# Performance work log

Hardware: AMD Instinct MI355X
Metric: run time of the kernel (lower is better)

## Reference

```python
import math
import jax, jax.numpy as jnp
import numpy as np

N, T, D, H, DH = 4, 2048, 1024, 16, 64
CAP = 30.0
EPS = 1e-5


def _layernorm(x, g, b):
    m = jnp.mean(x, axis=-1, keepdims=True)
    v = jnp.mean(jnp.square(x - m), axis=-1, keepdims=True)
    return (x - m) * jax.lax.rsqrt(v + EPS) * g + b


def _rope(x):
    # x: [N, H, t, d]; interleaved rotary (rotary-embedding-torch style), theta=10000
    t, d = x.shape[2], x.shape[3]
    inv_freq = 1.0 / (10000.0 ** (jnp.arange(0, d, 2, dtype=jnp.float32) / d))
    ang = jnp.arange(t, dtype=jnp.float32)[:, None] * inv_freq[None, :]  # [t, d/2]
    cos, sin = jnp.cos(ang), jnp.sin(ang)
    x1, x2 = x[..., 0::2], x[..., 1::2]
    r1 = x1 * cos - x2 * sin
    r2 = x1 * sin + x2 * cos
    return jnp.stack([r1, r2], axis=-1).reshape(x.shape)


def setup_inputs() -> dict:
    key = jax.random.key(0)
    ks = jax.random.split(key, 8)
    s = 0.02
    lengths = jax.random.randint(ks[6], (N,), T // 2, T + 1).astype(jnp.int32)
    key_padding_mask = jnp.arange(T)[None, :] >= lengths[:, None]  # True = pad
    attn_mask = jnp.triu(jnp.ones((T, T), dtype=bool), 1)  # causal: True = masked
    return {
        "x": jax.random.normal(ks[0], (N, T, D), jnp.float32),
        "ln_g": jnp.ones((D,), jnp.float32),
        "ln_b": jnp.zeros((D,), jnp.float32),
        "Wq": jax.random.normal(ks[1], (D, H * DH), jnp.float32) * s,
        "bq": jnp.zeros((H * DH,), jnp.float32),
        "Wk": jax.random.normal(ks[2], (D, H * DH), jnp.float32) * s,
        "bk": jnp.zeros((H * DH,), jnp.float32),
        "Wv": jax.random.normal(ks[3], (D, H * DH), jnp.float32) * s,
        "bv": jnp.zeros((H * DH,), jnp.float32),
        "Wo": jax.random.normal(ks[4], (H * DH, D), jnp.float32) * s,
        "bo": jnp.zeros((D,), jnp.float32),
        "key_padding_mask": key_padding_mask,
        "attn_mask": attn_mask,
        "key_value_sequence_lengths": lengths,
    }


def reference(x, ln_g, ln_b, Wq, bq, Wk, bk, Wv, bv, Wo, bo,
              key_padding_mask, attn_mask, key_value_sequence_lengths):
    n, t, _ = x.shape
    h = _layernorm(x, ln_g, ln_b)  # shared LN for q/k/v (self-attention)
    q = (h @ Wq + bq).reshape(n, t, H, DH).transpose(0, 2, 1, 3)  # [n,H,t,d]
    k = (h @ Wk + bk).reshape(n, t, H, DH).transpose(0, 2, 1, 3)
    v = (h @ Wv + bv).reshape(n, t, H, DH).transpose(0, 2, 1, 3)
    q = _rope(q)
    k = _rope(k)
    scores = jnp.einsum('bhtd,bhTd->bhtT', q, k) / math.sqrt(DH)
    scores = CAP * jnp.tanh(scores / CAP)  # tanh soft-cap
    mask = key_padding_mask[:, None, None, :] | attn_mask[None, None, :, :]
    scores = jnp.where(mask, -jnp.inf, scores)
    attn = jax.nn.softmax(scores, axis=-1)
    out = jnp.einsum('bhtT,bhTd->bhtd', attn, v)
    out = out.transpose(0, 2, 1, 3).reshape(n, t, H * DH)
    return out @ Wo + bo
```

## Files before the change

### kernel.cpp

```cpp
#include <hip/hip_runtime.h>
#include <hip/hip_bf16.h>

typedef unsigned short u16;
typedef unsigned int   u32;
typedef __bf16 bf16x8 __attribute__((ext_vector_type(8)));
typedef float  f32x4  __attribute__((ext_vector_type(4)));

#define NB 4
#define T_ 2048
#define D_ 1024
#define H_ 16
#define DH 64
#define M_ (NB * T_)
#define PSTR 72

__device__ __forceinline__ float bf2f(u16 u) {
    union { u32 i; float f; } v; v.i = ((u32)u) << 16; return v.f;
}
__device__ __forceinline__ u16 f2bf(float f) {
    union { float fl; u32 i; } v; v.fl = f;
    u32 r = v.i + 0x7fff + ((v.i >> 16) & 1);
    return (u16)(r >> 16);
}

__device__ __forceinline__ void gl_lds16(const u16* g, u16* l) {
    __builtin_amdgcn_global_load_lds((const __attribute__((address_space(1))) void*)g,
                                     (__attribute__((address_space(3))) void*)l,
                                     16, 0, 0);
}

__device__ __forceinline__ int detect_f32(const u16* p) {
    int weird = 0;
    const int lane = threadIdx.x & 63;
    #pragma unroll
    for (int i = 0; i < 4; ++i) {
        const u16 u = p[lane * 4 + i];
        const int e = (u >> 7) & 0xFF;
        weird += (e == 0xFF || (e >= 0x01 && e <= 0x3F) || (e >= 0xC0 && e <= 0xFE));
    }
    #pragma unroll
    for (int off = 32; off; off >>= 1) weird += __shfl_xor(weird, off);
    return weird >= 16;
}

__device__ __forceinline__ int read_len(const void* raw, int b) {
    const int* a32 = (const int*)raw;
    bool ok32 = true;
    #pragma unroll
    for (int i = 0; i < NB; ++i) {
        const int v = a32[i];
        if (v < 1 || v > T_) ok32 = false;
    }
    int v = ok32 ? a32[b] : (int)((const long long*)raw)[b];
    return min(max(v, 1), T_);
}

__global__ __launch_bounds__(256) void prep_kernel(const void* __restrict__ xraw,
                                                   const void* __restrict__ graw,
                                                   const void* __restrict__ braw,
                                                   u16* __restrict__ h,
                                                   const void* __restrict__ W0,
                                                   const void* __restrict__ W1,
                                                   const void* __restrict__ W2,
                                                   const void* __restrict__ W3,
                                                   u16* __restrict__ Wt0,
                                                   u16* __restrict__ Wt1,
                                                   u16* __restrict__ Wt2,
                                                   u16* __restrict__ Wt3,
                                                   float2* __restrict__ tab) {
    __shared__ __align__(16) u16 sh[64 * PSTR];
    const int bid = blockIdx.x;
    const int tid = threadIdx.x;

    if (bid < M_) {
        const int row = bid;
        const int isf = detect_f32((const u16*)xraw);
        float* red = (float*)sh;

        float xv[4];
        if (isf) {
            const float* xr = (const float*)xraw + (size_t)row * D_;
            *(float4*)xv = *(const float4*)&xr[tid * 4];
        } else {
            const u16* xr = (const u16*)xraw + (size_t)row * D_;
            u16 loc[4] __attribute__((aligned(8)));
            *(uint2*)loc = *(const uint2*)&xr[tid * 4];
            #pragma unroll
            for (int i = 0; i < 4; ++i) xv[i] = bf2f(loc[i]);
        }

        float s = xv[0] + xv[1] + xv[2] + xv[3];
        float q = xv[0]*xv[0] + xv[1]*xv[1] + xv[2]*xv[2] + xv[3]*xv[3];
        #pragma unroll
        for (int off = 32; off; off >>= 1) {
            s += __shfl_xor(s, off);
            q += __shfl_xor(q, off);
        }
        const int wave = tid >> 6, lane = tid & 63;
        if (lane == 0) { red[wave] = s; red[4 + wave] = q; }
        __syncthreads();
        s = red[0] + red[1] + red[2] + red[3];
        q = red[4] + red[5] + red[6] + red[7];

        const float mean = s * (1.0f / D_);
        const float var  = q * (1.0f / D_) - mean * mean;
        const float rs   = rsqrtf(var + 1e-5f);

        u16 o[4] __attribute__((aligned(8)));
        #pragma unroll
        for (int i = 0; i < 4; ++i) {
            const int c = tid * 4 + i;
            const float gv = isf ? ((const float*)graw)[c] : bf2f(((const u16*)graw)[c]);
            const float bv = isf ? ((const float*)braw)[c] : bf2f(((const u16*)braw)[c]);
            o[i] = f2bf((xv[i] - mean) * rs * gv + bv);
        }
        *(uint2*)&h[(size_t)row * D_ + tid * 4] = *(uint2*)o;
    } else if (bid < M_ + 1024) {
        const int w = bid - M_;
        const int z = w >> 8;
        const int t = w & 255;
        const void* Wraw = (z == 0) ? W0 : (z == 1) ? W1 : (z == 2) ? W2 : W3;
        u16* Wt          = (z == 0) ? Wt0 : (z == 1) ? Wt1 : (z == 2) ? Wt2 : Wt3;
        u16 (*tile)[PSTR] = (u16(*)[PSTR])sh;
        const int isf = detect_f32((const u16*)Wraw);
        const int n0 = (t & 15) * 64;
        const int k0 = (t >> 4) * 64;
        const int tr  = tid >> 2;
        const int tc  = (tid & 3) * 16;

        if (isf) {
            const float* W = (const float*)Wraw;
            #pragma unroll
            for (int i = 0; i < 16; ++i)
                tile[tc + i][tr] = f2bf(W[(size_t)(k0 + tr) * D_ + n0 + tc + i]);
        } else {
            const u16* W = (const u16*)Wraw;
            #pragma unroll
            for (int i = 0; i < 16; ++i)
                tile[tc + i][tr] = W[(size_t)(k0 + tr) * D_ + n0 + tc + i];
        }
        __syncthreads();
        *(uint4*)&Wt[(size_t)(n0 + tr) * D_ + k0 + tc]     = *(uint4*)&tile[tr][tc];
        *(uint4*)&Wt[(size_t)(n0 + tr) * D_ + k0 + tc + 8] = *(uint4*)&tile[tr][tc + 8];
    } else {
        const int gid = (bid - (M_ + 1024)) * 256 + tid;
        const int t = gid >> 5, i = gid & 31;
        const float inv = exp2f(-(float)i * 0.41524101186092f);
        const float ang = (float)t * inv;
        float sv, cv;
        sincosf(ang, &sv, &cv);
        tab[gid] = make_float2(cv, sv);
    }
}

__global__ __launch_bounds__(256) void wconv_kernel(const void* __restrict__ Wraw,
                                                    u16* __restrict__ Wt) {
    __shared__ u16 tile[64][PSTR];
    const int isf = detect_f32((const u16*)Wraw);
    const int n0 = blockIdx.x * 64;
    const int k0 = blockIdx.y * 64;
    const int tid = threadIdx.x;
    const int tr  = tid >> 2;
    const int tc  = (tid & 3) * 16;

    if (isf) {
        const float* W = (const float*)Wraw;
        #pragma unroll
        for (int i = 0; i < 16; ++i)
            tile[tc + i][tr] = f2bf(W[(size_t)(k0 + tr) * D_ + n0 + tc + i]);
    } else {
        const u16* W = (const u16*)Wraw;
        #pragma unroll
        for (int i = 0; i < 16; ++i)
            tile[tc + i][tr] = W[(size_t)(k0 + tr) * D_ + n0 + tc + i];
    }
    __syncthreads();
    *(uint4*)&Wt[(size_t)(n0 + tr) * D_ + k0 + tc]     = *(uint4*)&tile[tr][tc];
    *(uint4*)&Wt[(size_t)(n0 + tr) * D_ + k0 + tc + 8] = *(uint4*)&tile[tr][tc + 8];
}

__global__ __launch_bounds__(256) void vtrans_kernel(const u16* __restrict__ vtmp,
                                                     u16* __restrict__ vt) {
    __shared__ u16 tile[64][PSTR];
    const int bh = blockIdx.y;
    const int b  = bh >> 4;
    const int hh = bh & 15;
    const int t0 = blockIdx.x * 64;
    const int tid = threadIdx.x;
    const int tr  = tid >> 2;
    const int tc  = (tid & 3) * 16;

    #pragma unroll
    for (int i = 0; i < 16; ++i)
        tile[tc + i][tr] = vtmp[(size_t)(b * T_ + t0 + tr) * D_ + hh * DH + tc + i];
    __syncthreads();
    u16* dst = vt + (size_t)bh * DH * T_ + (size_t)tr * T_ + t0;
    *(uint4*)&dst[tc]     = *(uint4*)&tile[tr][tc];
    *(uint4*)&dst[tc + 8] = *(uint4*)&tile[tr][tc + 8];
}

__global__ __launch_bounds__(256) void qkv_kernel(const u16* __restrict__ A,
                                                  const u16* __restrict__ Wt3,
                                                  const void* __restrict__ Braw,
                                                  const void* __restrict__ bqr,
                                                  const void* __restrict__ bkr,
                                                  const void* __restrict__ bvr,
                                                  u16* __restrict__ qo,
                                                  u16* __restrict__ ko,
                                                  u16* __restrict__ vo,
                                                  const float2* __restrict__ tab) {
    __shared__ __align__(16) u16 As[128 * 64];
    __shared__ __align__(16) u16 Bs[128 * 64];

    const int tid   = threadIdx.x;
    const int wave  = tid >> 6;
    const int lane  = tid & 63;
    const int quad  = lane >> 4;
    const int lr    = lane & 15;
    const int ntile = blockIdx.x * 128;
    const int mtile = blockIdx.y * 128;
    const int seg   = ntile >> 10;

    const int isf = detect_f32((const u16*)Braw);

    const int srow = wave * 8 + (lane >> 3);
    const int sc   = (((lane & 7) ^ (lane >> 3)) * 8);
    const u16* aP = A   + (size_t)(mtile + srow) * D_ + sc;
    const u16* bP = Wt3 + (size_t)(ntile + srow) * D_ + sc;
    u16* aL = As + (wave * 8) * 64;
    u16* bL = Bs + (wave * 8) * 64;

    const int mbase = (wave >> 1) * 64;
    const int nbase = (wave & 1) * 64;

    f32x4 acc[4][4];
    #pragma unroll
    for (int m = 0; m < 4; ++m)
        #pragma unroll
        for (int n = 0; n < 4; ++n)
            acc[m][n] = (f32x4){0.f, 0.f, 0.f, 0.f};

    for (int k0 = 0; k0 < D_; k0 += 64) {
        #pragma unroll
        for (int j = 0; j < 4; ++j) {
            gl_lds16(aP + (size_t)(j * 32) * D_ + k0, aL + (j * 32) * 64);
            gl_lds16(bP + (size_t)(j * 32) * D_ + k0, bL + (j * 32) * 64);
        }
        __syncthreads();

        #pragma unroll
        for (int c = 0; c < 2; ++c) {
            bf16x8 af[4], bfr[4];
            #pragma unroll
            for (int m = 0; m < 4; ++m) {
                const int row = mbase + m * 16 + lr;
                af[m] = *(const bf16x8*)&As[row * 64 + (((c << 2) | quad) ^ (row & 7)) * 8];
            }
            #pragma unroll
            for (int n = 0; n < 4; ++n) {
                const int row = nbase + n * 16 + lr;
                bfr[n] = *(const bf16x8*)&Bs[row * 64 + (((c << 2) | quad) ^ (row & 7)) * 8];
            }
            #pragma unroll
            for (int m = 0; m < 4; ++m)
                #pragma unroll
                for (int n = 0; n < 4; ++n)
                    acc[m][n] = __builtin_amdgcn_mfma_f32_16x16x32_bf16(af[m], bfr[n], acc[m][n], 0, 0, 0);
        }
        __syncthreads();
    }

    const void* biasraw = (seg == 0) ? bqr : (seg == 1) ? bkr : bvr;
    u16* out            = (seg == 0) ? qo  : (seg == 1) ? ko  : vo;
    const int nloc = (ntile & 1023) + nbase;

    #pragma unroll
    for (int m = 0; m < 4; ++m) {
        #pragma unroll
        for (int n = 0; n < 4; ++n) {
            const int ncl = nloc + n * 16 + lr;
            const float bv = isf ? ((const float*)biasraw)[ncl]
                                 : bf2f(((const u16*)biasraw)[ncl]);
            #pragma unroll
            for (int r = 0; r < 4; ++r) {
                const int mrow = mtile + mbase + m * 16 + quad * 4 + r;
                float v = acc[m][n][r] + bv;
                if (seg < 2) {
                    const float other = __shfl_xor(v, 1);
                    const int d = ncl & (DH - 1);
                    const int t = mrow & (T_ - 1);
                    const float2 cs = tab[t * 32 + (d >> 1)];
                    v = (d & 1) ? (other * cs.y + v * cs.x) : (v * cs.x - other * cs.y);
                }
                out[(size_t)mrow * D_ + ncl] = f2bf(v);
            }
        }
    }
}

__global__ __launch_bounds__(256) void gemm128_kernel(const u16* __restrict__ A,
                                                      const u16* __restrict__ Bt,
                                                      const void* __restrict__ Braw,
                                                      const void* __restrict__ biasraw,
                                                      void* __restrict__ out,
                                                      const int mode) {
    __shared__ __align__(16) u16 As[128 * 64];
    __shared__ __align__(16) u16 Bs[128 * 64];

    const int tid   = threadIdx.x;
    const int wave  = tid >> 6;
    const int lane  = tid & 63;
    const int quad  = lane >> 4;
    const int lr    = lane & 15;
    const int ntile = blockIdx.x * 128;
    const int mtile = blockIdx.y * 128;

    const int isf = detect_f32((const u16*)Braw);

    const int srow = wave * 8 + (lane >> 3);
    const int sc   = (((lane & 7) ^ (lane >> 3)) * 8);
    const u16* aP = A  + (size_t)(mtile + srow) * D_ + sc;
    const u16* bP = Bt + (size_t)(ntile + srow) * D_ + sc;
    u16* aL = As + (wave * 8) * 64;
    u16* bL = Bs + (wave * 8) * 64;

    const int mbase = (wave >> 1) * 64;
    const int nbase = (wave & 1) * 64;

    f32x4 acc[4][4];
    #pragma unroll
    for (int m = 0; m < 4; ++m)
        #pragma unroll
        for (int n = 0; n < 4; ++n)
            acc[m][n] = (f32x4){0.f, 0.f, 0.f, 0.f};

    for (int k0 = 0; k0 < D_; k0 += 64) {
        #pragma unroll
        for (int j = 0; j < 4; ++j) {
            gl_lds16(aP + (size_t)(j * 32) * D_ + k0, aL + (j * 32) * 64);
            gl_lds16(bP + (size_t)(j * 32) * D_ + k0, bL + (j * 32) * 64);
        }
        __syncthreads();

        #pragma unroll
        for (int c = 0; c < 2; ++c) {
            bf16x8 af[4], bfr[4];
            #pragma unroll
            for (int m = 0; m < 4; ++m) {
                const int row = mbase + m * 16 + lr;
                af[m] = *(const bf16x8*)&As[row * 64 + (((c << 2) | quad) ^ (row & 7)) * 8];
            }
            #pragma unroll
            for (int n = 0; n < 4; ++n) {
                const int row = nbase + n * 16 + lr;
                bfr[n] = *(const bf16x8*)&Bs[row * 64 + (((c << 2) | quad) ^ (row & 7)) * 8];
            }
            #pragma unroll
            for (int m = 0; m < 4; ++m)
                #pragma unroll
                for (int n = 0; n < 4; ++n)
                    acc[m][n] = __builtin_amdgcn_mfma_f32_16x16x32_bf16(af[m], bfr[n], acc[m][n], 0, 0, 0);
        }
        __syncthreads();
    }

    #pragma unroll
    for (int m = 0; m < 4; ++m) {
        #pragma unroll
        for (int n = 0; n < 4; ++n) {
            const int ncol = ntile + nbase + n * 16 + lr;
            const float bv = isf ? ((const float*)biasraw)[ncol]
                                 : bf2f(((const u16*)biasraw)[ncol]);
            #pragma unroll
            for (int r = 0; r < 4; ++r) {
                const int mrow = mtile + mbase + m * 16 + quad * 4 + r;
                float v = acc[m][n][r] + bv;
                if (mode == 2) {
                    const float other = __shfl_xor(v, 1);
                    const int d = ncol & (DH - 1);
                    const int t = mrow & (T_ - 1);
                    const int i = d >> 1;
                    const float inv = exp2f(-(float)i * 0.41524101186092f);
                    const float ang = (float)t * inv;
                    float sv, cv;
                    __sincosf(ang, &sv, &cv);
                    v = (d & 1) ? (other * sv + v * cv) : (v * cv - other * sv);
                }
                const int d  = ncol & (DH - 1);
                const int hh = ncol >> 6;
                const int t  = mrow & (T_ - 1);
                const int bb = mrow >> 11;
                if (mode == 0) {
                    if (isf) ((float*)out)[(size_t)mrow * D_ + ncol] = v;
                    else     ((u16*)out)[(size_t)mrow * D_ + ncol] = f2bf(v);
                } else if (mode == 1) {
                    ((u16*)out)[(((size_t)(bb * H_ + hh) * DH) + d) * T_ + t] = f2bf(v);
                } else {
                    ((u16*)out)[(((size_t)(bb * H_ + hh) * T_) + t) * DH + d] = f2bf(v);
                }
            }
        }
    }
}

__global__ __launch_bounds__(256) void gemm_kernel(const u16* __restrict__ A,
                                                   const void* __restrict__ Braw,
                                                   const void* __restrict__ biasraw,
                                                   void* __restrict__ out,
                                                   const int mode) {
    __shared__ __align__(16) u16 As[128 * 32];
    __shared__ __align__(16) u16 Bs[64 * 32];

    const int tid   = threadIdx.x;
    const int ntile = blockIdx.x * 64;
    const int mtile = blockIdx.y * 128;
    const int wave  = tid >> 6;
    const int lane  = tid & 63;
    const int quad  = lane >> 4;
    const int lr    = lane & 15;

    const int isf = detect_f32((const u16*)Braw);
    const float* Bf = (const float*)Braw;
    const u16*   Bu = (const u16*)Braw;

    f32x4 acc[2][4];
    #pragma unroll
    for (int s = 0; s < 2; ++s)
        #pragma unroll
        for (int n = 0; n < 4; ++n)
            acc[s][n] = (f32x4){0.f, 0.f, 0.f, 0.f};

    const int ar  = tid >> 1;
    const int akb = (tid & 1) * 16;
    const int bn  = tid & 63;
    const int bkb = (tid >> 6) * 8;
    const u16* Arow = A + (size_t)(mtile + ar) * D_ + akb;
    const size_t bcol0 = (size_t)bkb * D_ + ntile + bn;

    for (int k0 = 0; k0 < D_; k0 += 32) {
        *(uint4*)&As[ar * 32 + akb]     = *(const uint4*)(Arow + k0);
        *(uint4*)&As[ar * 32 + akb + 8] = *(const uint4*)(Arow + k0 + 8);
        {
            u16 tmp[8] __attribute__((aligned(16)));
            if (isf) {
                #pragma unroll
                for (int j = 0; j < 8; ++j) tmp[j] = f2bf(Bf[bcol0 + (size_t)(k0 + j) * D_]);
            } else {
                #pragma unroll
                for (int j = 0; j < 8; ++j) tmp[j] = Bu[bcol0 + (size_t)(k0 + j) * D_];
            }
            *(uint4*)&Bs[bn * 32 + bkb] = *(uint4*)tmp;
        }
        __syncthreads();

        const int mbase = wave * 32;
        bf16x8 af0 = *(const bf16x8*)&As[(mbase +      lr) * 32 + quad * 8];
        bf16x8 af1 = *(const bf16x8*)&As[(mbase + 16 + lr) * 32 + quad * 8];
        #pragma unroll
        for (int nt = 0; nt < 4; ++nt) {
            bf16x8 bf = *(const bf16x8*)&Bs[(nt * 16 + lr) * 32 + quad * 8];
            acc[0][nt] = __builtin_amdgcn_mfma_f32_16x16x32_bf16(af0, bf, acc[0][nt], 0, 0, 0);
            acc[1][nt] = __builtin_amdgcn_mfma_f32_16x16x32_bf16(af1, bf, acc[1][nt], 0, 0, 0);
        }
        __syncthreads();
    }

    #pragma unroll
    for (int s2 = 0; s2 < 2; ++s2) {
        #pragma unroll
        for (int nt = 0; nt < 4; ++nt) {
            const int ncol = ntile + nt * 16 + lr;
            const float bv = isf ? ((const float*)biasraw)[ncol]
                                 : bf2f(((const u16*)biasraw)[ncol]);
            #pragma unroll
            for (int r = 0; r < 4; ++r) {
                const int mrow = mtile + wave * 32 + s2 * 16 + quad * 4 + r;
                float v = acc[s2][nt][r] + bv;
                if (mode == 2) {
                    const float other = __shfl_xor(v, 1);
                    const int d = ncol & (DH - 1);
                    const int t = mrow & (T_ - 1);
                    const int i = d >> 1;
                    const float inv = exp2f(-(float)i * 0.41524101186092f);
                    const float ang = (float)t * inv;
                    const float cv = cosf(ang), sv = sinf(ang);
                    v = (d & 1) ? (other * sv + v * cv) : (v * cv - other * sv);
                }
                const int d  = ncol & (DH - 1);
                const int hh = ncol >> 6;
                const int t  = mrow & (T_ - 1);
                const int bb = mrow >> 11;
                if (mode == 0) {
                    if (isf) ((float*)out)[(size_t)mrow * D_ + ncol] = v;
                    else     ((u16*)out)[(size_t)mrow * D_ + ncol] = f2bf(v);
                } else if (mode == 1) {
                    ((u16*)out)[(((size_t)(bb * H_ + hh) * DH) + d) * T_ + t] = f2bf(v);
                } else {
                    ((u16*)out)[(((size_t)(bb * H_ + hh) * T_) + t) * DH + d] = f2bf(v);
                }
            }
        }
    }
}

__global__ __launch_bounds__(256) void attn_kernel(const u16* __restrict__ Q,
                                                   const u16* __restrict__ K,
                                                   const u16* __restrict__ Vt,
                                                   const void* __restrict__ lensraw,
                                                   u16* __restrict__ ctx,
                                                   const int rowmajor) {
    __shared__ __align__(16) u16 Ps[64 * PSTR];
    __shared__ __align__(16) u16 Ks[64 * PSTR];
    __shared__ __align__(16) u16 Vts[64 * PSTR];

    const int tid  = threadIdx.x;
    const int wave = tid >> 6;
    const int lane = tid & 63;
    const int quad = lane >> 4;
    const int lr   = lane & 15;

    const int bid = blockIdx.x;
    const int swz = (bid & 7) * 128 + (bid >> 3);
    const int qx  = swz & 15;
    const int bh  = swz >> 4;
    const int qs_lo = qx * 64;
    const int qs_hi = (31 - qx) * 64;
    const int b    = bh >> 4;
    const int hh   = bh & 15;
    const int len  = read_len(lensraw, b);

    const size_t qkstride = rowmajor ? (size_t)D_ : (size_t)DH;
    const size_t qkoff    = rowmajor ? ((size_t)b * T_ * D_ + hh * DH)
                                     : ((size_t)bh * T_ * DH);
    const u16* Qp = Q + qkoff;
    const u16* Kp = K + qkoff;
    const u16* Vb = Vt + (size_t)bh * DH * T_;

    const int srow = tid >> 2;
    const int scb  = (tid & 3) * 16;

    *(uint4*)&Ps[srow * PSTR + scb]     = *(const uint4*)&Qp[(size_t)(qs_lo + srow) * qkstride + scb];
    *(uint4*)&Ps[srow * PSTR + scb + 8] = *(const uint4*)&Qp[(size_t)(qs_lo + srow) * qkstride + scb + 8];
    const bf16x8 qaL0 = *(const bf16x8*)&Ps[(wave * 16 + lr) * PSTR + quad * 8];
    const bf16x8 qaL1 = *(const bf16x8*)&Ps[(wave * 16 + lr) * PSTR + 32 + quad * 8];
    *(uint4*)&Ps[srow * PSTR + scb]     = *(const uint4*)&Qp[(size_t)(qs_hi + srow) * qkstride + scb];
    *(uint4*)&Ps[srow * PSTR + scb + 8] = *(const uint4*)&Qp[(size_t)(qs_hi + srow) * qkstride + scb + 8];
    const bf16x8 qaH0 = *(const bf16x8*)&Ps[(wave * 16 + lr) * PSTR + quad * 8];
    const bf16x8 qaH1 = *(const bf16x8*)&Ps[(wave * 16 + lr) * PSTR + 32 + quad * 8];

    {
        uint4 k0 = *(const uint4*)&Kp[(size_t)srow * qkstride + scb];
        uint4 k1 = *(const uint4*)&Kp[(size_t)srow * qkstride + scb + 8];
        uint4 v0 = *(const uint4*)&Vb[(size_t)srow * T_ + scb];
        uint4 v1 = *(const uint4*)&Vb[(size_t)srow * T_ + scb + 8];
        *(uint4*)&Ks[srow * PSTR + scb]      = k0;
        *(uint4*)&Ks[srow * PSTR + scb + 8]  = k1;
        *(uint4*)&Vts[srow * PSTR + scb]     = v0;
        *(uint4*)&Vts[srow * PSTR + scb + 8] = v1;
    }
    __syncthreads();

    f32x4 accL[4], accH[4];
    float lL[4] = {0.f, 0.f, 0.f, 0.f};
    float lH[4] = {0.f, 0.f, 0.f, 0.f};
    #pragma unroll
    for (int nt = 0; nt < 4; ++nt) {
        accL[nt] = (f32x4){0.f, 0.f, 0.f, 0.f};
        accH[nt] = (f32x4){0.f, 0.f, 0.f, 0.f};
    }

    const int ktnL = min(qs_lo + 63, len - 1) / 64 + 1;
    const int ktnH = min(qs_hi + 63, len - 1) / 64 + 1;
    const int prow = wave * 16 + quad * 4;

    const float C1 = 1.44269504f / 120.0f;
    const float C2 = -60.0f * 1.44269504f;

    uint4 kr0, kr1, vr0, vr1;
    for (int kt = 0; kt < ktnH; ++kt) {
        const int ks = kt * 64;
        const bool havenext = (kt + 1 < ktnH);
        const bool lo_act   = (kt < ktnL);

        if (havenext) {
            const int ns = ks + 64;
            kr0 = *(const uint4*)&Kp[(size_t)(ns + srow) * qkstride + scb];
            kr1 = *(const uint4*)&Kp[(size_t)(ns + srow) * qkstride + scb + 8];
            vr0 = *(const uint4*)&Vb[(size_t)srow * T_ + ns + scb];
            vr1 = *(const uint4*)&Vb[(size_t)srow * T_ + ns + scb + 8];
        }

        {
            f32x4 s[4];
            #pragma unroll
            for (int nt = 0; nt < 4; ++nt) s[nt] = (f32x4){0.f, 0.f, 0.f, 0.f};
            __builtin_amdgcn_s_setprio(1);
            #pragma unroll
            for (int nt = 0; nt < 4; ++nt) {
                bf16x8 kb0 = *(const bf16x8*)&Ks[(nt * 16 + lr) * PSTR + quad * 8];
                bf16x8 kb1 = *(const bf16x8*)&Ks[(nt * 16 + lr) * PSTR + 32 + quad * 8];
                s[nt] = __builtin_amdgcn_mfma_f32_16x16x32_bf16(qaH0, kb0, s[nt], 0, 0, 0);
                s[nt] = __builtin_amdgcn_mfma_f32_16x16x32_bf16(qaH1, kb1, s[nt], 0, 0, 0);
            }
            __builtin_amdgcn_s_setprio(0);

            const bool need_mask = (ks == qs_hi) || (ks + 63 >= len);
            if (!need_mask) {
                #pragma unroll
                for (int r = 0; r < 4; ++r) {
                    #pragma unroll
                    for (int nt = 0; nt < 4; ++nt) {
                        const float z = __builtin_amdgcn_exp2f(s[nt][r] * C1);
                        const float p = __builtin_amdgcn_exp2f(C2 * __builtin_amdgcn_rcpf(z + 1.0f));
                        lH[r] += p;
                        Ps[(prow + r) * PSTR + nt * 16 + lr] = f2bf(p);
                    }
                }
            } else {
                #pragma unroll
                for (int r = 0; r < 4; ++r) {
                    const int trow = qs_hi + prow + r;
                    #pragma unroll
                    for (int nt = 0; nt < 4; ++nt) {
                        const float z = __builtin_amdgcn_exp2f(s[nt][r] * C1);
                        float p = __builtin_amdgcn_exp2f(C2 * __builtin_amdgcn_rcpf(z + 1.0f));
                        const int col = ks + nt * 16 + lr;
                        p = (col > trow || col >= len) ? 0.f : p;
                        lH[r] += p;
                        Ps[(prow + r) * PSTR + nt * 16 + lr] = f2bf(p);
                    }
                }
            }
            bf16x8 pa0 = *(const bf16x8*)&Ps[(wave * 16 + lr) * PSTR + quad * 8];
            bf16x8 pa1 = *(const bf16x8*)&Ps[(wave * 16 + lr) * PSTR + 32 + quad * 8];
            __builtin_amdgcn_s_setprio(1);
            #pragma unroll
            for (int nt = 0; nt < 4; ++nt) {
                bf16x8 vb0 = *(const bf16x8*)&Vts[(nt * 16 + lr) * PSTR + quad * 8];
                bf16x8 vb1 = *(const bf16x8*)&Vts[(nt * 16 + lr) * PSTR + 32 + quad * 8];
                accH[nt] = __builtin_amdgcn_mfma_f32_16x16x32_bf16(pa0, vb0, accH[nt], 0, 0, 0);
                accH[nt] = __builtin_amdgcn_mfma_f32_16x16x32_bf16(pa1, vb1, accH[nt], 0, 0, 0);
            }
            __builtin_amdgcn_s_setprio(0);
        }

        if (lo_act) {
            f32x4 s[4];
            #pragma unroll
            for (int nt = 0; nt < 4; ++nt) s[nt] = (f32x4){0.f, 0.f, 0.f, 0.f};
            __builtin_amdgcn_s_setprio(1);
            #pragma unroll
            for (int nt = 0; nt < 4; ++nt) {
                bf16x8 kb0 = *(const bf16x8*)&Ks[(nt * 16 + lr) * PSTR + quad * 8];
                bf16x8 kb1 = *(const bf16x8*)&Ks[(nt * 16 + lr) * PSTR + 32 + quad * 8];
                s[nt] = __builtin_amdgcn_mfma_f32_16x16x32_bf16(qaL0, kb0, s[nt], 0, 0, 0);
                s[nt] = __builtin_amdgcn_mfma_f32_16x16x32_bf16(qaL1, kb1, s[nt], 0, 0, 0);
            }
            __builtin_amdgcn_s_setprio(0);

            const bool need_mask = (ks == qs_lo) || (ks + 63 >= len);
            if (!need_mask) {
                #pragma unroll
                for (int r = 0; r < 4; ++r) {
                    #pragma unroll
                    for (int nt = 0; nt < 4; ++nt) {
                        const float z = __builtin_amdgcn_exp2f(s[nt][r] * C1);
                        const float p = __builtin_amdgcn_exp2f(C2 * __builtin_amdgcn_rcpf(z + 1.0f));
                        lL[r] += p;
                        Ps[(prow + r) * PSTR + nt * 16 + lr] = f2bf(p);
                    }
                }
            } else {
                #pragma unroll
                for (int r = 0; r < 4; ++r) {
                    const int trow = qs_lo + prow + r;
                    #pragma unroll
                    for (int nt = 0; nt < 4; ++nt) {
                        const float z = __builtin_amdgcn_exp2f(s[nt][r] * C1);
                        float p = __builtin_amdgcn_exp2f(C2 * __builtin_amdgcn_rcpf(z + 1.0f));
                        const int col = ks + nt * 16 + lr;
                        p = (col > trow || col >= len) ? 0.f : p;
                        lL[r] += p;
                        Ps[(prow + r) * PSTR + nt * 16 + lr] = f2bf(p);
                    }
                }
            }
            bf16x8 pa0 = *(const bf16x8*)&Ps[(wave * 16 + lr) * PSTR + quad * 8];
            bf16x8 pa1 = *(const bf16x8*)&Ps[(wave * 16 + lr) * PSTR + 32 + quad * 8];
            __builtin_amdgcn_s_setprio(1);
            #pragma unroll
            for (int nt = 0; nt < 4; ++nt) {
                bf16x8 vb0 = *(const bf16x8*)&Vts[(nt * 16 + lr) * PSTR + quad * 8];
                bf16x8 vb1 = *(const bf16x8*)&Vts[(nt * 16 + lr) * PSTR + 32 + quad * 8];
                accL[nt] = __builtin_amdgcn_mfma_f32_16x16x32_bf16(pa0, vb0, accL[nt], 0, 0, 0);
                accL[nt] = __builtin_amdgcn_mfma_f32_16x16x32_bf16(pa1, vb1, accL[nt], 0, 0, 0);
            }
            __builtin_amdgcn_s_setprio(0);
        }

        if (havenext) {
            __syncthreads();
            *(uint4*)&Ks[srow * PSTR + scb]      = kr0;
            *(uint4*)&Ks[srow * PSTR + scb + 8]  = kr1;
            *(uint4*)&Vts[srow * PSTR + scb]     = vr0;
            *(uint4*)&Vts[srow * PSTR + scb + 8] = vr1;
            __syncthreads();
        }
    }

    #pragma unroll
    for (int r = 0; r < 4; ++r) {
        float ll = lL[r], lh = lH[r];
        #pragma unroll
        for (int off = 1; off < 16; off <<= 1) {
            ll += __shfl_xor(ll, off);
            lh += __shfl_xor(lh, off);
        }
        const float invL = (ll > 0.f) ? (1.0f / ll) : 0.f;
        const float invH = (lh > 0.f) ? (1.0f / lh) : 0.f;
        const int qrow = prow + r;
        #pragma unroll
        for (int nt = 0; nt < 4; ++nt) {
            ctx[(size_t)(b * T_ + qs_lo + qrow) * D_ + hh * DH + nt * 16 + lr] =
                f2bf(accL[nt][r] * invL);
            ctx[(size_t)(b * T_ + qs_hi + qrow) * D_ + hh * DH + nt * 16 + lr] =
                f2bf(accH[nt][r] * invH);
        }
    }
}

extern "C" void kernel_launch(void* const* d_in, const int* in_sizes, int n_in,
                              void* d_out, int out_size, void* d_ws, size_t ws_size,
                              hipStream_t stream) {
    u16* h = (u16*)d_ws;
    const size_t MD = (size_t)M_ * D_;
    const size_t WD = (size_t)D_ * D_;
    u16* q  = h + MD;
    u16* k  = q + MD;
    u16* vt = k + MD;
    const bool havewt  = ws_size >= (4 * MD + 4 * WD) * sizeof(u16);
    const bool havebig = ws_size >= (5 * MD + 4 * WD) * sizeof(u16)
                                    + (size_t)T_ * 32 * sizeof(float2);
    u16* wtq = havewt ? (vt + MD)  : nullptr;
    u16* wtk = havewt ? (wtq + WD) : nullptr;
    u16* wtv = havewt ? (wtk + WD) : nullptr;
    u16* wto = havewt ? (wtv + WD) : nullptr;
    u16* vtmp = havebig ? (wto + WD) : nullptr;
    float2* tab = havebig ? (float2*)(vtmp + MD) : nullptr;

    if (havebig) {
        prep_kernel<<<M_ + 1024 + 256, 256, 0, stream>>>(
            d_in[0], d_in[1], d_in[2], h,
            d_in[3], d_in[5], d_in[7], d_in[9], wtq, wtk, wtv, wto, tab);

        qkv_kernel<<<dim3(3 * D_ / 128, M_ / 128), 256, 0, stream>>>(
            h, wtq, d_in[3], d_in[4], d_in[6], d_in[8], q, k, vtmp, tab);

        vtrans_kernel<<<dim3(T_ / 64, NB * H_), 256, 0, stream>>>(vtmp, vt);

        attn_kernel<<<(T_ / 128) * NB * H_, 256, 0, stream>>>(q, k, vt, d_in[13], h, 1);

        gemm128_kernel<<<dim3(D_ / 128, M_ / 128), 256, 0, stream>>>(
            h, wto, d_in[9], d_in[10], d_out, 0);
    } else if (havewt) {
        prep_kernel<<<M_, 256, 0, stream>>>(
            d_in[0], d_in[1], d_in[2], h,
            d_in[3], d_in[5], d_in[7], d_in[9], wtq, wtk, wtv, wto, nullptr);
        dim3 wgrid(D_ / 64, D_ / 64);
        wconv_kernel<<<wgrid, 256, 0, stream>>>(d_in[3], wtq);
        wconv_kernel<<<wgrid, 256, 0, stream>>>(d_in[5], wtk);
        wconv_kernel<<<wgrid, 256, 0, stream>>>(d_in[7], wtv);
        wconv_kernel<<<wgrid, 256, 0, stream>>>(d_in[9], wto);

        dim3 g128(D_ / 128, M_ / 128);
        gemm128_kernel<<<g128, 256, 0, stream>>>(h, wtq, d_in[3], d_in[4], q, 2);
        gemm128_kernel<<<g128, 256, 0, stream>>>(h, wtk, d_in[5], d_in[6], k, 2);
        gemm128_kernel<<<g128, 256, 0, stream>>>(h, wtv, d_in[7], d_in[8], vt, 1);

        attn_kernel<<<(T_ / 128) * NB * H_, 256, 0, stream>>>(q, k, vt, d_in[13], h, 0);

        gemm128_kernel<<<g128, 256, 0, stream>>>(h, wto, d_in[9], d_in[10], d_out, 0);
    } else {
        prep_kernel<<<M_, 256, 0, stream>>>(
            d_in[0], d_in[1], d_in[2], h,
            d_in[3], d_in[5], d_in[7], d_in[9], nullptr, nullptr, nullptr, nullptr, nullptr);
        dim3 ggrid(D_ / 64, M_ / 128);
        gemm_kernel<<<ggrid, 256, 0, stream>>>(h, d_in[3], d_in[4], q, 2);
        gemm_kernel<<<ggrid, 256, 0, stream>>>(h, d_in[5], d_in[6], k, 2);
        gemm_kernel<<<ggrid, 256, 0, stream>>>(h, d_in[7], d_in[8], vt, 1);

        attn_kernel<<<(T_ / 128) * NB * H_, 256, 0, stream>>>(q, k, vt, d_in[13], h, 0);

        gemm_kernel<<<ggrid, 256, 0, stream>>>(h, d_in[9], d_in[10], d_out, 0);
    }
}
```

Baseline: 389.1 us.

## Interleave hi/lo attention tiles and remap GEMM blocks per XCD

In the attention kernel, the QK^T MFMAs for the high and low query tiles are now issued together, then both softmax passes run, then both PV products run. The low tile writes to a second P buffer in shared memory. This gives the scheduler more independent MFMA and exp work to interleave, at the cost of extra LDS and registers. The QKV and output GEMMs move to a 1D grid with a block-index swizzle over 8 XCDs, so that neighbouring tiles share L2.

```diff
diff --git a/kernel.cpp b/kernel.cpp
--- a/kernel.cpp
+++ b/kernel.cpp
@@ -217,8 +217,11 @@
     const int lane  = tid & 63;
     const int quad  = lane >> 4;
     const int lr    = lane & 15;
-    const int ntile = blockIdx.x * 128;
-    const int mtile = blockIdx.y * 128;
+
+    const int bid = blockIdx.x;
+    const int wg  = (bid & 7) * 192 + (bid >> 3);
+    const int ntile = (wg % 24) * 128;
+    const int mtile = (wg / 24) * 128;
     const int seg   = ntile >> 10;
 
     const int isf = detect_f32((const u16*)Braw);
@@ -303,6 +306,7 @@
                                                       const void* __restrict__ Braw,
                                                       const void* __restrict__ biasraw,
                                                       void* __restrict__ out,
+                                                      const int nx,
                                                       const int mode) {
     __shared__ __align__(16) u16 As[128 * 64];
     __shared__ __align__(16) u16 Bs[128 * 64];
@@ -312,8 +316,12 @@
     const int lane  = tid & 63;
     const int quad  = lane >> 4;
     const int lr    = lane & 15;
-    const int ntile = blockIdx.x * 128;
-    const int mtile = blockIdx.y * 128;
+
+    const int bid = blockIdx.x;
+    const int cpx = (nx * (M_ / 128)) >> 3;
+    const int wg  = (bid & 7) * cpx + (bid >> 3);
+    const int ntile = (wg % nx) * 128;
+    const int mtile = (wg / nx) * 128;
 
     const int isf = detect_f32((const u16*)Braw);
 
@@ -510,6 +518,7 @@
                                                    u16* __restrict__ ctx,
                                                    const int rowmajor) {
     __shared__ __align__(16) u16 Ps[64 * PSTR];
+    __shared__ __align__(16) u16 Ps2[64 * PSTR];
     __shared__ __align__(16) u16 Ks[64 * PSTR];
     __shared__ __align__(16) u16 Vts[64 * PSTR];
 
@@ -590,27 +599,34 @@
             vr1 = *(const uint4*)&Vb[(size_t)srow * T_ + ns + scb + 8];
         }
 
+        f32x4 sH[4], sL[4];
+        #pragma unroll
+        for (int nt = 0; nt < 4; ++nt) {
+            sH[nt] = (f32x4){0.f, 0.f, 0.f, 0.f};
+            sL[nt] = (f32x4){0.f, 0.f, 0.f, 0.f};
+        }
+        __builtin_amdgcn_s_setprio(1);
+        #pragma unroll
+        for (int nt = 0; nt < 4; ++nt) {
+            bf16x8 kb0 = *(const bf16x8*)&Ks[(nt * 16 + lr) * PSTR + quad * 8];
+            bf16x8 kb1 = *(const bf16x8*)&Ks[(nt * 16 + lr) * PSTR + 32 + quad * 8];
+            sH[nt] = __builtin_amdgcn_mfma_f32_16x16x32_bf16(qaH0, kb0, sH[nt], 0, 0, 0);
+            sH[nt] = __builtin_amdgcn_mfma_f32_16x16x32_bf16(qaH1, kb1, sH[nt], 0, 0, 0);
+            if (lo_act) {
+                sL[nt] = __builtin_amdgcn_mfma_f32_16x16x32_bf16(qaL0, kb0, sL[nt], 0, 0, 0);
+                sL[nt] = __builtin_amdgcn_mfma_f32_16x16x32_bf16(qaL1, kb1, sL[nt], 0, 0, 0);
+            }
+        }
+        __builtin_amdgcn_s_setprio(0);
+
         {
-            f32x4 s[4];
-            #pragma unroll
-            for (int nt = 0; nt < 4; ++nt) s[nt] = (f32x4){0.f, 0.f, 0.f, 0.f};
-            __builtin_amdgcn_s_setprio(1);
-            #pragma unroll
-            for (int nt = 0; nt < 4; ++nt) {
-                bf16x8 kb0 = *(const bf16x8*)&Ks[(nt * 16 + lr) * PSTR + quad * 8];
-                bf16x8 kb1 = *(const bf16x8*)&Ks[(nt * 16 + lr) * PSTR + 32 + quad * 8];
-                s[nt] = __builtin_amdgcn_mfma_f32_16x16x32_bf16(qaH0, kb0, s[nt], 0, 0, 0);
-                s[nt] = __builtin_amdgcn_mfma_f32_16x16x32_bf16(qaH1, kb1, s[nt], 0, 0, 0);
-            }
-            __builtin_amdgcn_s_setprio(0);
-
-            const bool need_mask = (ks == qs_hi) || (ks + 63 >= len);
-            if (!need_mask) {
+            const bool mH = (ks == qs_hi) || (ks + 63 >= len);
+            if (!mH) {
                 #pragma unroll
                 for (int r = 0; r < 4; ++r) {
                     #pragma unroll
                     for (int nt = 0; nt < 4; ++nt) {
-                        const float z = __builtin_amdgcn_exp2f(s[nt][r] * C1);
+                        const float z = __builtin_amdgcn_exp2f(sH[nt][r] * C1);
                         const float p = __builtin_amdgcn_exp2f(C2 * __builtin_amdgcn_rcpf(z + 1.0f));
                         lH[r] += p;
                         Ps[(prow + r) * PSTR + nt * 16 + lr] = f2bf(p);
@@ -622,7 +638,7 @@
                     const int trow = qs_hi + prow + r;
                     #pragma unroll
                     for (int nt = 0; nt < 4; ++nt) {
-                        const float z = __builtin_amdgcn_exp2f(s[nt][r] * C1);
+                        const float z = __builtin_amdgcn_exp2f(sH[nt][r] * C1);
                         float p = __builtin_amdgcn_exp2f(C2 * __builtin_amdgcn_rcpf(z + 1.0f));
                         const int col = ks + nt * 16 + lr;
                         p = (col > trow || col >= len) ? 0.f : p;
@@ -631,43 +647,18 @@
                     }
                 }
             }
-            bf16x8 pa0 = *(const bf16x8*)&Ps[(wave * 16 + lr) * PSTR + quad * 8];
-            bf16x8 pa1 = *(const bf16x8*)&Ps[(wave * 16 + lr) * PSTR + 32 + quad * 8];
-            __builtin_amdgcn_s_setprio(1);
-            #pragma unroll
-            for (int nt = 0; nt < 4; ++nt) {
-                bf16x8 vb0 = *(const bf16x8*)&Vts[(nt * 16 + lr) * PSTR + quad * 8];
-                bf16x8 vb1 = *(const bf16x8*)&Vts[(nt * 16 + lr) * PSTR + 32 + quad * 8];
-                accH[nt] = __builtin_amdgcn_mfma_f32_16x16x32_bf16(pa0, vb0, accH[nt], 0, 0, 0);
-                accH[nt] = __builtin_amdgcn_mfma_f32_16x16x32_bf16(pa1, vb1, accH[nt], 0, 0, 0);
-            }
-            __builtin_amdgcn_s_setprio(0);
-        }
-
+        }
         if (lo_act) {
-            f32x4 s[4];
-            #pragma unroll
-            for (int nt = 0; nt < 4; ++nt) s[nt] = (f32x4){0.f, 0.f, 0.f, 0.f};
-            __builtin_amdgcn_s_setprio(1);
-            #pragma unroll
-            for (int nt = 0; nt < 4; ++nt) {
-                bf16x8 kb0 = *(const bf16x8*)&Ks[(nt * 16 + lr) * PSTR + quad * 8];
-                bf16x8 kb1 = *(const bf16x8*)&Ks[(nt * 16 + lr) * PSTR + 32 + quad * 8];
-                s[nt] = __builtin_amdgcn_mfma_f32_16x16x32_bf16(qaL0, kb0, s[nt], 0, 0, 0);
-                s[nt] = __builtin_amdgcn_mfma_f32_16x16x32_bf16(qaL1, kb1, s[nt], 0, 0, 0);
-            }
-            __builtin_amdgcn_s_setprio(0);
-
-            const bool need_mask = (ks == qs_lo) || (ks + 63 >= len);
-            if (!need_mask) {
+            const bool mL = (ks == qs_lo) || (ks + 63 >= len);
+            if (!mL) {
                 #pragma unroll
                 for (int r = 0; r < 4; ++r) {
                     #pragma unroll
                     for (int nt = 0; nt < 4; ++nt) {
-                        const float z = __builtin_amdgcn_exp2f(s[nt][r] * C1);
+                        const float z = __builtin_amdgcn_exp2f(sL[nt][r] * C1);
                         const float p = __builtin_amdgcn_exp2f(C2 * __builtin_amdgcn_rcpf(z + 1.0f));
                         lL[r] += p;
-                        Ps[(prow + r) * PSTR + nt * 16 + lr] = f2bf(p);
+                        Ps2[(prow + r) * PSTR + nt * 16 + lr] = f2bf(p);
                     }
                 }
             } else {
@@ -676,27 +667,34 @@
                     const int trow = qs_lo + prow + r;
                     #pragma unroll
                     for (int nt = 0; nt < 4; ++nt) {
-                        const float z = __builtin_amdgcn_exp2f(s[nt][r] * C1);
+                        const float z = __builtin_amdgcn_exp2f(sL[nt][r] * C1);
                         float p = __builtin_amdgcn_exp2f(C2 * __builtin_amdgcn_rcpf(z + 1.0f));
                         const int col = ks + nt * 16 + lr;
                         p = (col > trow || col >= len) ? 0.f : p;
                         lL[r] += p;
-                        Ps[(prow + r) * PSTR + nt * 16 + lr] = f2bf(p);
+                        Ps2[(prow + r) * PSTR + nt * 16 + lr] = f2bf(p);
                     }
                 }
             }
-            bf16x8 pa0 = *(const bf16x8*)&Ps[(wave * 16 + lr) * PSTR + quad * 8];
-            bf16x8 pa1 = *(const bf16x8*)&Ps[(wave * 16 + lr) * PSTR + 32 + quad * 8];
-            __builtin_amdgcn_s_setprio(1);
-            #pragma unroll
-            for (int nt = 0; nt < 4; ++nt) {
-                bf16x8 vb0 = *(const bf16x8*)&Vts[(nt * 16 + lr) * PSTR + quad * 8];
-                bf16x8 vb1 = *(const bf16x8*)&Vts[(nt * 16 + lr) * PSTR + 32 + quad * 8];
-                accL[nt] = __builtin_amdgcn_mfma_f32_16x16x32_bf16(pa0, vb0, accL[nt], 0, 0, 0);
-                accL[nt] = __builtin_amdgcn_mfma_f32_16x16x32_bf16(pa1, vb1, accL[nt], 0, 0, 0);
-            }
-            __builtin_amdgcn_s_setprio(0);
-        }
+        }
+
+        bf16x8 paH0 = *(const bf16x8*)&Ps[(wave * 16 + lr) * PSTR + quad * 8];
+        bf16x8 paH1 = *(const bf16x8*)&Ps[(wave * 16 + lr) * PSTR + 32 + quad * 8];
+        bf16x8 paL0 = *(const bf16x8*)&Ps2[(wave * 16 + lr) * PSTR + quad * 8];
+        bf16x8 paL1 = *(const bf16x8*)&Ps2[(wave * 16 + lr) * PSTR + 32 + quad * 8];
+        __builtin_amdgcn_s_setprio(1);
+        #pragma unroll
+        for (int nt = 0; nt < 4; ++nt) {
+            bf16x8 vb0 = *(const bf16x8*)&Vts[(nt * 16 + lr) * PSTR + quad * 8];
+            bf16x8 vb1 = *(const bf16x8*)&Vts[(nt * 16 + lr) * PSTR + 32 + quad * 8];
+            accH[nt] = __builtin_amdgcn_mfma_f32_16x16x32_bf16(paH0, vb0, accH[nt], 0, 0, 0);
+            accH[nt] = __builtin_amdgcn_mfma_f32_16x16x32_bf16(paH1, vb1, accH[nt], 0, 0, 0);
+            if (lo_act) {
+                accL[nt] = __builtin_amdgcn_mfma_f32_16x16x32_bf16(paL0, vb0, accL[nt], 0, 0, 0);
+                accL[nt] = __builtin_amdgcn_mfma_f32_16x16x32_bf16(paL1, vb1, accL[nt], 0, 0, 0);
+            }
+        }
+        __builtin_amdgcn_s_setprio(0);
 
         if (havenext) {
             __syncthreads();
@@ -753,15 +751,15 @@
             d_in[0], d_in[1], d_in[2], h,
             d_in[3], d_in[5], d_in[7], d_in[9], wtq, wtk, wtv, wto, tab);
 
-        qkv_kernel<<<dim3(3 * D_ / 128, M_ / 128), 256, 0, stream>>>(
+        qkv_kernel<<<1536, 256, 0, stream>>>(
             h, wtq, d_in[3], d_in[4], d_in[6], d_in[8], q, k, vtmp, tab);
 
         vtrans_kernel<<<dim3(T_ / 64, NB * H_), 256, 0, stream>>>(vtmp, vt);
 
         attn_kernel<<<(T_ / 128) * NB * H_, 256, 0, stream>>>(q, k, vt, d_in[13], h, 1);
 
-        gemm128_kernel<<<dim3(D_ / 128, M_ / 128), 256, 0, stream>>>(
-            h, wto, d_in[9], d_in[10], d_out, 0);
+        gemm128_kernel<<<8 * (M_ / 128), 256, 0, stream>>>(
+            h, wto, d_in[9], d_in[10], d_out, 8, 0);
     } else if (havewt) {
         prep_kernel<<<M_, 256, 0, stream>>>(
             d_in[0], d_in[1], d_in[2], h,
@@ -772,14 +770,14 @@
         wconv_kernel<<<wgrid, 256, 0, stream>>>(d_in[7], wtv);
         wconv_kernel<<<wgrid, 256, 0, stream>>>(d_in[9], wto);
 
-        dim3 g128(D_ / 128, M_ / 128);
-        gemm128_kernel<<<g128, 256, 0, stream>>>(h, wtq, d_in[3], d_in[4], q, 2);
-        gemm128_kernel<<<g128, 256, 0, stream>>>(h, wtk, d_in[5], d_in[6], k, 2);
-        gemm128_kernel<<<g128, 256, 0, stream>>>(h, wtv, d_in[7], d_in[8], vt, 1);
+        const int g1 = 8 * (M_ / 128);
+        gemm128_kernel<<<g1, 256, 0, stream>>>(h, wtq, d_in[3], d_in[4], q, 8, 2);
+        gemm128_kernel<<<g1, 256, 0, stream>>>(h, wtk, d_in[5], d_in[6], k, 8, 2);
+        gemm128_kernel<<<g1, 256, 0, stream>>>(h, wtv, d_in[7], d_in[8], vt, 8, 1);
 
         attn_kernel<<<(T_ / 128) * NB * H_, 256, 0, stream>>>(q, k, vt, d_in[13], h, 0);
 
-        gemm128_kernel<<<g128, 256, 0, stream>>>(h, wto, d_in[9], d_in[10], d_out, 0);
+        gemm128_kernel<<<g1, 256, 0, stream>>>(h, wto, d_in[9], d_in[10], d_out, 8, 0);
     } else {
         prep_kernel<<<M_, 256, 0, stream>>>(
             d_in[0], d_in[1], d_in[2], h,
```

Measured after the change: 381.4 us. -2.0%, faster.
